# Kernel optimization log

Measured on AMD Instinct MI355X. Metric: run time of the kernel, lower is better.

The kernel has to match this reference:

```python
import jax, jax.numpy as jnp
import numpy as np

B, D, V = 128, 4096, 32000


def setup_inputs() -> dict:
    key = jax.random.key(0)
    k1, k2, k3, k4 = jax.random.split(key, 4)
    hidden_states = jax.random.normal(k1, (B, D), dtype=jnp.float32)
    embd_weight = jax.random.normal(k2, (V, D), dtype=jnp.float32) * 0.02
    # per-row temperature in [0.5, 1.5), top_p in [0.7, 1.0)
    temperature = jax.random.uniform(k3, (B,), jnp.float32, 0.5, 1.5)
    top_p = jax.random.uniform(k4, (B,), jnp.float32, 0.7, 1.0)
    return {"hidden_states": hidden_states, "embd_weight": embd_weight,
            "temperature": temperature, "top_p": top_p}


def _topp_logits(hidden_states, embd_weight, temperature, top_p):
    # [B, V] logits via tied LM head
    logits = jnp.einsum('bd,vd->bv', hidden_states, embd_weight)
    logits = logits / temperature[:, None]
    # descending sort (matches torch sort(descending=True))
    order = jnp.argsort(-logits, axis=-1)                    # [B, V]
    sorted_logits = jnp.take_along_axis(logits, order, axis=-1)
    sorted_probs = jax.nn.softmax(sorted_logits, axis=-1)
    cum = jnp.cumsum(sorted_probs, axis=-1)
    # mask tokens whose preceding cumulative prob already exceeds top_p
    mask = (cum - sorted_probs) > top_p[:, None]
    sorted_logits = jnp.where(mask, -jnp.inf, sorted_logits)
    inv = jnp.argsort(order, axis=-1)                        # undo the sort
    return jnp.take_along_axis(sorted_logits, inv, axis=-1)


def reference(hidden_states, embd_weight, temperature, top_p):
    logits = _topp_logits(hidden_states, embd_weight, temperature, top_p)
    probs = jax.nn.softmax(logits.astype(jnp.float32), axis=-1)
    # multinomial(num_samples=1) == categorical sample per row (fixed key for determinism)
    ids = jax.random.categorical(jax.random.key(42), jnp.log(probs), axis=-1)
    return ids
```

## Files before the change

### kernel.cpp

```cpp
#include <hip/hip_runtime.h>
#include <math.h>

#define B_ 128
#define D_ 4096
#define V_ 32000

#define BN 64
#define BK 32
#define KSTEPS (D_ / BK)
#define ASTEP_BYTES (128 * BK * 2 * 3)
#define WS_LDS_BYTES (3 * 4 * 4 * 16 * 16)
#define WS_LDS_OFF ASTEP_BYTES

typedef __attribute__((ext_vector_type(8))) short short8;
typedef __attribute__((ext_vector_type(4))) float floatx4;

__device__ __forceinline__ unsigned short bf16_rne(float x) {
  unsigned u = __float_as_uint(x);
  u += 0x7FFFu + ((u >> 16) & 1u);
  return (unsigned short)(u >> 16);
}
__device__ __forceinline__ float bf16_to_f(unsigned short h) {
  return __uint_as_float(((unsigned)h) << 16);
}

__device__ __forceinline__ void threefry2x32_0_42(unsigned& x0, unsigned& x1) {
  const unsigned k0 = 0u;
  const unsigned k1 = 42u;
  const unsigned k2 = 0u ^ 42u ^ 0x1BD11BDAu;
  x0 += k0; x1 += k1;
#define TF_R(r) { x0 += x1; x1 = (x1 << (r)) | (x1 >> (32 - (r))); x1 ^= x0; }
#define TF_G0 TF_R(13) TF_R(15) TF_R(26) TF_R(6)
#define TF_G1 TF_R(17) TF_R(29) TF_R(16) TF_R(24)
  TF_G0; x0 += k1; x1 += k2 + 1u;
  TF_G1; x0 += k2; x1 += k0 + 2u;
  TF_G0; x0 += k0; x1 += k1 + 3u;
  TF_G1; x0 += k1; x1 += k2 + 4u;
  TF_G0; x0 += k2; x1 += k0 + 5u;
#undef TF_G1
#undef TF_G0
#undef TF_R
}

__device__ __forceinline__ float gumbel_from_bits(unsigned bits) {
  float f = __uint_as_float((bits >> 9) | 0x3F800000u) - 1.0f;
  float u = fmaxf(f, 1.17549435e-38f);
  return -logf(-logf(u));
}

__global__ __launch_bounds__(256) void asplit_kernel(const float* __restrict__ A,
                                                     unsigned short* __restrict__ Asp) {
  const int t = blockIdx.x * 256 + threadIdx.x;
  const int m_glob = t >> 9;
  const int koct = t & 511;
  const int sk = koct >> 2, quad = koct & 3;
  const int mt = m_glob >> 4, ml = m_glob & 15;
  const float* src = A + (size_t)m_glob * D_ + koct * 8;
  short8 h0, h1, h2;
#pragma unroll
  for (int kk = 0; kk < 8; kk++) {
    const float x = src[kk];
    const unsigned short a0 = bf16_rne(x);
    const float r1 = x - bf16_to_f(a0);
    const unsigned short a1 = bf16_rne(r1);
    const float r2 = r1 - bf16_to_f(a1);
    const unsigned short a2 = bf16_rne(r2);
    h0[kk] = (short)a0; h1[kk] = (short)a1; h2[kk] = (short)a2;
  }
  unsigned short* dst = Asp + (size_t)sk * (ASTEP_BYTES / 2);
  const int base = ((mt * 4 + quad) * 16 + ml) * 8;
  const int sstride = 8 * 4 * 16 * 8;
  *(short8*)(dst + base) = h0;
  *(short8*)(dst + base + sstride) = h1;
  *(short8*)(dst + base + 2 * sstride) = h2;
}

__global__ __launch_bounds__(256) void gemm_mfma(const unsigned short* __restrict__ Asp,
                                                 const float* __restrict__ W,
                                                 const float* __restrict__ temp,
                                                 float* __restrict__ L) {
  __shared__ unsigned char lds[ASTEP_BYTES + WS_LDS_BYTES];
  const int tid = threadIdx.x;
  const int vblock = blockIdx.x * BN;
  const int wave = tid >> 6, lane = tid & 63;
  const int quad = lane >> 4, ml = lane & 15;
  const int wm = wave >> 1, wn = wave & 1;

  const int wv = tid >> 2;
  const int wko = tid & 3;
  const float* wsrc = W + (size_t)(vblock + wv) * D_ + wko * 8;
  const int wnt = wv >> 4, wvl = wv & 15;
  const int wbase0 = WS_LDS_OFF + (((0 * 4 + wnt) * 4 + wko) * 16 + wvl) * 16;
  const int wsstride = 4 * 4 * 16 * 16;

  floatx4 acc[4][2];
#pragma unroll
  for (int i = 0; i < 4; i++)
#pragma unroll
    for (int j = 0; j < 2; j++) acc[i][j] = (floatx4){0.f, 0.f, 0.f, 0.f};

  for (int st = 0; st < KSTEPS; st++) {
    __syncthreads();
    const unsigned char* abase = (const unsigned char*)(Asp + (size_t)st * (ASTEP_BYTES / 2));
#pragma unroll
    for (int i = 0; i < 6; i++) {
      const int off = (i * 256 + tid) * 16;
      __builtin_amdgcn_global_load_lds(
          (const __attribute__((address_space(1))) unsigned int*)(abase + off),
          (__attribute__((address_space(3))) unsigned int*)(&lds[off]), 16, 0, 0);
    }
    {
      const float* wp = wsrc + st * BK;
      const float4 wa = *(const float4*)(wp);
      const float4 wb = *(const float4*)(wp + 4);
      const float x[8] = {wa.x, wa.y, wa.z, wa.w, wb.x, wb.y, wb.z, wb.w};
      short8 w0, w1, w2;
#pragma unroll
      for (int kk = 0; kk < 8; kk++) {
        const unsigned short b0 = bf16_rne(x[kk]);
        const float r1 = x[kk] - bf16_to_f(b0);
        const unsigned short b1 = bf16_rne(r1);
        const float r2 = r1 - bf16_to_f(b1);
        const unsigned short b2 = bf16_rne(r2);
        w0[kk] = (short)b0; w1[kk] = (short)b1; w2[kk] = (short)b2;
      }
      *(short8*)(&lds[wbase0]) = w0;
      *(short8*)(&lds[wbase0 + wsstride]) = w1;
      *(short8*)(&lds[wbase0 + 2 * wsstride]) = w2;
    }
    __syncthreads();

    short8 af[3][4];
#pragma unroll
    for (int s = 0; s < 3; s++)
#pragma unroll
      for (int i = 0; i < 4; i++) {
        const int mt = wm * 4 + i;
        af[s][i] = *(const short8*)(&lds[(((s * 8 + mt) * 4 + quad) * 16 + ml) * 16]);
      }
    short8 wf[3][2];
#pragma unroll
    for (int s = 0; s < 3; s++)
#pragma unroll
      for (int j = 0; j < 2; j++) {
        const int nt = wn * 2 + j;
        wf[s][j] = *(const short8*)(&lds[WS_LDS_OFF + (((s * 4 + nt) * 4 + quad) * 16 + ml) * 16]);
      }

#pragma unroll
    for (int i = 0; i < 4; i++)
#pragma unroll
      for (int j = 0; j < 2; j++) {
        acc[i][j] = __builtin_amdgcn_mfma_f32_16x16x32_bf16(af[0][i], wf[0][j], acc[i][j], 0, 0, 0);
        acc[i][j] = __builtin_amdgcn_mfma_f32_16x16x32_bf16(af[0][i], wf[1][j], acc[i][j], 0, 0, 0);
        acc[i][j] = __builtin_amdgcn_mfma_f32_16x16x32_bf16(af[1][i], wf[0][j], acc[i][j], 0, 0, 0);
        acc[i][j] = __builtin_amdgcn_mfma_f32_16x16x32_bf16(af[1][i], wf[1][j], acc[i][j], 0, 0, 0);
        acc[i][j] = __builtin_amdgcn_mfma_f32_16x16x32_bf16(af[0][i], wf[2][j], acc[i][j], 0, 0, 0);
        acc[i][j] = __builtin_amdgcn_mfma_f32_16x16x32_bf16(af[2][i], wf[0][j], acc[i][j], 0, 0, 0);
      }
  }

#pragma unroll
  for (int i = 0; i < 4; i++)
#pragma unroll
    for (int j = 0; j < 2; j++) {
      const int col = vblock + (wn * 2 + j) * 16 + ml;
#pragma unroll
      for (int r = 0; r < 4; r++) {
        const int row = wm * 64 + i * 16 + quad * 4 + r;
        L[(size_t)row * V_ + col] = acc[i][j][r] / temp[row];
      }
    }
}

#define NBINS 8192
#define SHIFT 17
#define CAP 2048

__device__ __forceinline__ float blockSum1024(float x, float* redf) {
#pragma unroll
  for (int o = 32; o > 0; o >>= 1) x += __shfl_down(x, o);
  const int w = threadIdx.x >> 6;
  __syncthreads();
  if ((threadIdx.x & 63) == 0) redf[w] = x;
  __syncthreads();
  if (threadIdx.x == 0) {
    float t = redf[0];
    for (int k = 1; k < 16; k++) t += redf[k];
    redf[16] = t;
  }
  __syncthreads();
  return redf[16];
}

__device__ __forceinline__ float blockMax1024(float x, float* redf) {
#pragma unroll
  for (int o = 32; o > 0; o >>= 1) x = fmaxf(x, __shfl_down(x, o));
  const int w = threadIdx.x >> 6;
  __syncthreads();
  if ((threadIdx.x & 63) == 0) redf[w] = x;
  __syncthreads();
  if (threadIdx.x == 0) {
    float t = redf[0];
    for (int k = 1; k < 16; k++) t = fmaxf(t, redf[k]);
    redf[16] = t;
  }
  __syncthreads();
  return redf[16];
}

__global__ __launch_bounds__(1024) void sampler_kernel(const float* __restrict__ L,
                                                       const float* __restrict__ top_p,
                                                       int* __restrict__ out) {
  __shared__ float hist[NBINS];
  __shared__ float listE[CAP];
  __shared__ int cnt;
  __shared__ float redf[20];
  __shared__ int redi[16];
  const int b = blockIdx.x, tid = threadIdx.x;
  const float* l = L + (size_t)b * V_;

  for (int i = tid; i < NBINS; i += 1024) hist[i] = 0.f;
  if (tid == 0) cnt = 0;
  __syncthreads();

  float mx = -INFINITY;
  for (int v = tid; v < V_; v += 1024) mx = fmaxf(mx, l[v]);
  mx = blockMax1024(mx, redf);

  float s = 0.f;
  for (int v = tid; v < V_; v += 1024) {
    const float e = expf(l[v] - mx);
    s += e;
    unsigned bin = __float_as_uint(e) >> SHIFT;
    if (bin >= NBINS) bin = NBINS - 1;
    atomicAdd(&hist[bin], e);
  }
  const float S = blockSum1024(s, redf);
  const float ps = top_p[b] * S;

  int lo = -1, hi = NBINS - 1;
  while (hi - lo > 1) {
    const int mid = (lo + hi) >> 1;
    float a = 0.f;
    for (int i = tid; i < NBINS; i += 1024)
      if (i > mid) a += hist[i];
    a = blockSum1024(a, redf);
    if (a <= ps) hi = mid; else lo = mid;
  }
  const int beta = hi;
  float cumAbove;
  {
    float a = 0.f;
    for (int i = tid; i < NBINS; i += 1024)
      if (i > beta) a += hist[i];
    cumAbove = blockSum1024(a, redf);
  }

  for (int v = tid; v < V_; v += 1024) {
    const float e = expf(l[v] - mx);
    unsigned bin = __float_as_uint(e) >> SHIFT;
    if (bin >= NBINS) bin = NBINS - 1;
    if ((int)bin == beta) {
      const int p = atomicAdd(&cnt, 1);
      if (p < CAP) listE[p] = e;
    }
  }
  __syncthreads();
  const int n = cnt;

  long long blo = ((long long)beta << SHIFT) - 1;
  long long bhi = ((long long)(beta + 1)) << SHIFT;
  if (n <= CAP) {
    while (bhi - blo > 1) {
      const long long mid = (blo + bhi) >> 1;
      const float t = __uint_as_float((unsigned)mid);
      float a = 0.f;
      for (int i = tid; i < n; i += 1024) {
        const float e = listE[i];
        if (e > t) a += e;
      }
      a = cumAbove + blockSum1024(a, redf);
      if (a <= ps) bhi = mid; else blo = mid;
    }
  } else {
    while (bhi - blo > 1) {
      const long long mid = (blo + bhi) >> 1;
      const float t = __uint_as_float((unsigned)mid);
      float a = 0.f;
      for (int v = tid; v < V_; v += 1024) {
        const float e = expf(l[v] - mx);
        unsigned bin = __float_as_uint(e) >> SHIFT;
        if (bin >= NBINS) bin = NBINS - 1;
        if ((int)bin == beta && e > t) a += e;
      }
      a = cumAbove + blockSum1024(a, redf);
      if (a <= ps) bhi = mid; else blo = mid;
    }
  }
  const unsigned c = (unsigned)bhi;

  float best = -INFINITY;
  int bi = 0x7FFFFFFF;
  for (int v = tid; v < V_; v += 1024) {
    const float lv = l[v];
    const float e = expf(lv - mx);
    if (__float_as_uint(e) >= c) {
      unsigned x0 = 0u, x1 = (unsigned)(b * V_ + v);
      threefry2x32_0_42(x0, x1);
      const float sc = lv + gumbel_from_bits(x0 ^ x1);
      if (sc > best) { best = sc; bi = v; }
    }
  }
#pragma unroll
  for (int o = 32; o > 0; o >>= 1) {
    const float t = __shfl_down(best, o);
    const int j = __shfl_down(bi, o);
    if (t > best || (t == best && j < bi)) { best = t; bi = j; }
  }
  const int w = tid >> 6;
  __syncthreads();
  if ((tid & 63) == 0) { redf[w] = best; redi[w] = bi; }
  __syncthreads();
  if (tid == 0) {
    float bs = redf[0];
    int bidx = redi[0];
    for (int k = 1; k < 16; k++)
      if (redf[k] > bs || (redf[k] == bs && redi[k] < bidx)) { bs = redf[k]; bidx = redi[k]; }
    out[b] = bidx;
  }
}

extern "C" void kernel_launch(void* const* d_in, const int* in_sizes, int n_in,
                              void* d_out, int out_size, void* d_ws, size_t ws_size,
                              hipStream_t stream) {
  (void)in_sizes; (void)n_in; (void)out_size; (void)ws_size;
  const float* A = (const float*)d_in[0];
  const float* W = (const float*)d_in[1];
  const float* temp = (const float*)d_in[2];
  const float* topp = (const float*)d_in[3];
  int* out = (int*)d_out;

  char* base = (char*)d_ws;
  float* L = (float*)base;
  unsigned short* Asp = (unsigned short*)(base + (size_t)B_ * V_ * 4);

  asplit_kernel<<<dim3(256), dim3(256), 0, stream>>>(A, Asp);
  gemm_mfma<<<dim3(V_ / BN), dim3(256), 0, stream>>>(Asp, W, temp, L);
  sampler_kernel<<<dim3(B_), dim3(1024), 0, stream>>>(L, topp, out);
}
```

Measured before the change: 877.6 us.

## Replace bf16x3 split GEMM with scaled fp16x2 split and prefetch W

Switches the fp32-emulating GEMM from a three-way bf16 split (six MFMAs per tile) to a two-way fp16 split with power-of-two prescaling (four MFMAs), cutting matrix-core work, LDS footprint and A-split traffic by about a third. It also software-prefetches the next W slice into registers before the barrier so global loads overlap the MFMAs. The fp16 split has less dynamic range and relies on the scales keeping the inputs in range, which risks precision loss or overflow for other input distributions and could flip sampled tokens near ties.

```diff
diff --git a/kernel.cpp b/kernel.cpp
--- a/kernel.cpp
+++ b/kernel.cpp
@@ -8,21 +8,18 @@
 #define BN 64
 #define BK 32
 #define KSTEPS (D_ / BK)
-#define ASTEP_BYTES (128 * BK * 2 * 3)
-#define WS_LDS_BYTES (3 * 4 * 4 * 16 * 16)
+#define ASTEP_BYTES (128 * BK * 2 * 2)
+#define ASTEP_SHORTS (ASTEP_BYTES / 2)
+#define WS_LDS_BYTES (2 * 4 * 4 * 16 * 16)
 #define WS_LDS_OFF ASTEP_BYTES
 
+#define SCALE_A 256.0f
+#define SCALE_W 4096.0f
+#define DESCALE 9.5367431640625e-7f
+
 typedef __attribute__((ext_vector_type(8))) short short8;
+typedef __attribute__((ext_vector_type(8))) _Float16 half8;
 typedef __attribute__((ext_vector_type(4))) float floatx4;
-
-__device__ __forceinline__ unsigned short bf16_rne(float x) {
-  unsigned u = __float_as_uint(x);
-  u += 0x7FFFu + ((u >> 16) & 1u);
-  return (unsigned short)(u >> 16);
-}
-__device__ __forceinline__ float bf16_to_f(unsigned short h) {
-  return __uint_as_float(((unsigned)h) << 16);
-}
 
 __device__ __forceinline__ void threefry2x32_0_42(unsigned& x0, unsigned& x1) {
   const unsigned k0 = 0u;
@@ -56,23 +53,20 @@
   const int sk = koct >> 2, quad = koct & 3;
   const int mt = m_glob >> 4, ml = m_glob & 15;
   const float* src = A + (size_t)m_glob * D_ + koct * 8;
-  short8 h0, h1, h2;
+  half8 h0, h1;
 #pragma unroll
   for (int kk = 0; kk < 8; kk++) {
-    const float x = src[kk];
-    const unsigned short a0 = bf16_rne(x);
-    const float r1 = x - bf16_to_f(a0);
-    const unsigned short a1 = bf16_rne(r1);
-    const float r2 = r1 - bf16_to_f(a1);
-    const unsigned short a2 = bf16_rne(r2);
-    h0[kk] = (short)a0; h1[kk] = (short)a1; h2[kk] = (short)a2;
-  }
-  unsigned short* dst = Asp + (size_t)sk * (ASTEP_BYTES / 2);
+    const float x = src[kk] * SCALE_A;
+    const _Float16 a0 = (_Float16)x;
+    const float r1 = x - (float)a0;
+    const _Float16 a1 = (_Float16)r1;
+    h0[kk] = a0; h1[kk] = a1;
+  }
+  unsigned short* dst = Asp + (size_t)sk * ASTEP_SHORTS;
   const int base = ((mt * 4 + quad) * 16 + ml) * 8;
   const int sstride = 8 * 4 * 16 * 8;
-  *(short8*)(dst + base) = h0;
-  *(short8*)(dst + base + sstride) = h1;
-  *(short8*)(dst + base + 2 * sstride) = h2;
+  *(half8*)(dst + base) = h0;
+  *(half8*)(dst + base + sstride) = h1;
 }
 
 __global__ __launch_bounds__(256) void gemm_mfma(const unsigned short* __restrict__ Asp,
@@ -99,64 +93,66 @@
 #pragma unroll
     for (int j = 0; j < 2; j++) acc[i][j] = (floatx4){0.f, 0.f, 0.f, 0.f};
 
+  float4 wa = *(const float4*)(wsrc);
+  float4 wb = *(const float4*)(wsrc + 4);
+
   for (int st = 0; st < KSTEPS; st++) {
     __syncthreads();
-    const unsigned char* abase = (const unsigned char*)(Asp + (size_t)st * (ASTEP_BYTES / 2));
-#pragma unroll
-    for (int i = 0; i < 6; i++) {
+    const unsigned char* abase = (const unsigned char*)(Asp + (size_t)st * ASTEP_SHORTS);
+#pragma unroll
+    for (int i = 0; i < 4; i++) {
       const int off = (i * 256 + tid) * 16;
       __builtin_amdgcn_global_load_lds(
           (const __attribute__((address_space(1))) unsigned int*)(abase + off),
           (__attribute__((address_space(3))) unsigned int*)(&lds[off]), 16, 0, 0);
     }
     {
-      const float* wp = wsrc + st * BK;
-      const float4 wa = *(const float4*)(wp);
-      const float4 wb = *(const float4*)(wp + 4);
       const float x[8] = {wa.x, wa.y, wa.z, wa.w, wb.x, wb.y, wb.z, wb.w};
-      short8 w0, w1, w2;
+      half8 w0, w1;
 #pragma unroll
       for (int kk = 0; kk < 8; kk++) {
-        const unsigned short b0 = bf16_rne(x[kk]);
-        const float r1 = x[kk] - bf16_to_f(b0);
-        const unsigned short b1 = bf16_rne(r1);
-        const float r2 = r1 - bf16_to_f(b1);
-        const unsigned short b2 = bf16_rne(r2);
-        w0[kk] = (short)b0; w1[kk] = (short)b1; w2[kk] = (short)b2;
-      }
-      *(short8*)(&lds[wbase0]) = w0;
-      *(short8*)(&lds[wbase0 + wsstride]) = w1;
-      *(short8*)(&lds[wbase0 + 2 * wsstride]) = w2;
+        const float xs = x[kk] * SCALE_W;
+        const _Float16 b0 = (_Float16)xs;
+        const float r1 = xs - (float)b0;
+        const _Float16 b1 = (_Float16)r1;
+        w0[kk] = b0; w1[kk] = b1;
+      }
+      *(half8*)(&lds[wbase0]) = w0;
+      *(half8*)(&lds[wbase0 + wsstride]) = w1;
+    }
+    {
+      const int stn = (st + 1 < KSTEPS) ? st + 1 : st;
+      const float* wp = wsrc + (size_t)stn * BK;
+      wa = *(const float4*)(wp);
+      wb = *(const float4*)(wp + 4);
     }
     __syncthreads();
 
-    short8 af[3][4];
-#pragma unroll
-    for (int s = 0; s < 3; s++)
+    half8 af[2][4];
+#pragma unroll
+    for (int s = 0; s < 2; s++)
 #pragma unroll
       for (int i = 0; i < 4; i++) {
         const int mt = wm * 4 + i;
-        af[s][i] = *(const short8*)(&lds[(((s * 8 + mt) * 4 + quad) * 16 + ml) * 16]);
-      }
-    short8 wf[3][2];
-#pragma unroll
-    for (int s = 0; s < 3; s++)
+        af[s][i] = *(const half8*)(&lds[(((s * 8 + mt) * 4 + quad) * 16 + ml) * 16]);
+      }
+    half8 wf[2][2];
+#pragma unroll
+    for (int s = 0; s < 2; s++)
 #pragma unroll
       for (int j = 0; j < 2; j++) {
         const int nt = wn * 2 + j;
-        wf[s][j] = *(const short8*)(&lds[WS_LDS_OFF + (((s * 4 + nt) * 4 + quad) * 16 + ml) * 16]);
+        wf[s][j] = *(const half8*)(&lds[WS_LDS_OFF + (((s * 4 + nt) * 4 + quad) * 16 + ml) * 16]);
       }
 
 #pragma unroll
     for (int i = 0; i < 4; i++)
 #pragma unroll
       for (int j = 0; j < 2; j++) {
-        acc[i][j] = __builtin_amdgcn_mfma_f32_16x16x32_bf16(af[0][i], wf[0][j], acc[i][j], 0, 0, 0);
-        acc[i][j] = __builtin_amdgcn_mfma_f32_16x16x32_bf16(af[0][i], wf[1][j], acc[i][j], 0, 0, 0);
-        acc[i][j] = __builtin_amdgcn_mfma_f32_16x16x32_bf16(af[1][i], wf[0][j], acc[i][j], 0, 0, 0);
-        acc[i][j] = __builtin_amdgcn_mfma_f32_16x16x32_bf16(af[1][i], wf[1][j], acc[i][j], 0, 0, 0);
-        acc[i][j] = __builtin_amdgcn_mfma_f32_16x16x32_bf16(af[0][i], wf[2][j], acc[i][j], 0, 0, 0);
-        acc[i][j] = __builtin_amdgcn_mfma_f32_16x16x32_bf16(af[2][i], wf[0][j], acc[i][j], 0, 0, 0);
+        acc[i][j] = __builtin_amdgcn_mfma_f32_16x16x32_f16(af[0][i], wf[0][j], acc[i][j], 0, 0, 0);
+        acc[i][j] = __builtin_amdgcn_mfma_f32_16x16x32_f16(af[0][i], wf[1][j], acc[i][j], 0, 0, 0);
+        acc[i][j] = __builtin_amdgcn_mfma_f32_16x16x32_f16(af[1][i], wf[0][j], acc[i][j], 0, 0, 0);
+        acc[i][j] = __builtin_amdgcn_mfma_f32_16x16x32_f16(af[1][i], wf[1][j], acc[i][j], 0, 0, 0);
       }
   }
 
@@ -168,7 +164,7 @@
 #pragma unroll
       for (int r = 0; r < 4; r++) {
         const int row = wm * 64 + i * 16 + quad * 4 + r;
-        L[(size_t)row * V_ + col] = acc[i][j][r] / temp[row];
+        L[(size_t)row * V_ + col] = acc[i][j][r] * (DESCALE / temp[row]);
       }
     }
 }
```

Result: no change. 871.9 us (-0.6%).
